# Kernel tuning notes

Measured on AMD Instinct MI355X. Metric: run time of the kernel, lower is better.

## Reference

```python
import jax, jax.numpy as jnp
import numpy as np

B, L, D = 2, 2048, 1536
H = 12            # num_heads == num_key_value_heads
FDIM = 16         # feature_dim (per-head q/k dim)
HD = D // H       # head_dim = 128 (per-head v dim)
EPS = 1e-12
W_STD = 0.02


def setup_inputs() -> dict:
    key = jax.random.key(0)
    k0, k1, k2, k3, k4 = jax.random.split(key, 5)
    hidden_states = jax.random.normal(k0, (B, L, D), dtype=jnp.float32)
    Wq = jax.random.normal(k1, (D, H * FDIM), dtype=jnp.float32) * W_STD
    Wk = jax.random.normal(k2, (D, H * FDIM), dtype=jnp.float32) * W_STD
    Wv = jax.random.normal(k3, (D, H * HD), dtype=jnp.float32) * W_STD
    Wo = jax.random.normal(k4, (H * HD, D), dtype=jnp.float32) * W_STD
    return {"hidden_states": hidden_states, "Wq": Wq, "Wk": Wk, "Wv": Wv, "Wo": Wo}


def _split_heads(x, h):
    b, l, hd = x.shape
    return x.reshape(b, l, h, hd // h).transpose(0, 2, 1, 3)  # b h l d


def reference(hidden_states, Wq, Wk, Wv, Wo):
    b, l, _ = hidden_states.shape
    q = _split_heads(hidden_states @ Wq, H)  # [b,h,l,FDIM]
    k = _split_heads(hidden_states @ Wk, H)  # [b,h,l,FDIM]
    v = _split_heads(hidden_states @ Wv, H)  # [b,h,l,HD]

    # parallel_based(q, k, v, eps, use_scale=True, use_normalize=True)
    q = q * (FDIM ** -0.5)
    s = jnp.einsum('bhld,bhmd->bhlm', q, k)            # raw qk scores
    attn = 1.0 + s + 0.5 * s * s                        # 2nd-order Taylor of exp
    causal = jnp.tril(jnp.ones((l, l), dtype=bool))
    attn = jnp.where(causal, attn, 0.0)
    o = jnp.einsum('bhlm,bhmd->bhld', attn, v)          # [b,h,l,HD]
    z = attn.sum(axis=-1)                               # causal normalizer [b,h,l]
    o = o / (z[..., None] + EPS)

    o = o.transpose(0, 2, 1, 3).reshape(b, l, H * HD)   # b l (h d)
    return o @ Wo
```

## Files before the change

kernel.cpp:

```cpp
#include <hip/hip_runtime.h>
#include <hip/hip_bf16.h>

typedef short short8 __attribute__((ext_vector_type(8)));
typedef float f32x4  __attribute__((ext_vector_type(4)));
typedef unsigned int u32x4 __attribute__((ext_vector_type(4)));

union V16   { u32x4 v; short8 s; };
union U16x8 { u32x4 v; unsigned short u[8]; };
union FB4   { u32x4 v; float f[4]; };
union BF2U  { __hip_bfloat162 h; unsigned int u; };

__device__ inline unsigned short f2bf(float f) {
  union { float f; unsigned int u; } x; x.f = f;
  unsigned int u = x.u + 0x7fffu + ((x.u >> 16) & 1u);
  return (unsigned short)(u >> 16);
}

__device__ __forceinline__ int probe_fp32(const unsigned short* hs) {
  int bad = 0;
#pragma unroll
  for (int i = 0; i < 64; ++i) {
    unsigned int e = (hs[2 * i] >> 7) & 0xFFu;
    if (e >= 0xFEu || (e > 0u && e < 0x60u)) bad++;
  }
  return bad >= 6;
}

__device__ __forceinline__ void gl_lds16(const unsigned short* g, unsigned short* l) {
  __builtin_amdgcn_global_load_lds(
      (const __attribute__((address_space(1))) unsigned int*)g,
      (__attribute__((address_space(3))) unsigned int*)l, 16, 0, 0);
}

__global__ __launch_bounds__(256) void w_tr(const void* __restrict__ Wq,
                                            const void* __restrict__ Wk,
                                            const void* __restrict__ Wv,
                                            const void* __restrict__ Wo,
                                            const void* __restrict__ hs,
                                            unsigned short* __restrict__ WT,
                                            unsigned short* __restrict__ WoT,
                                            unsigned short* __restrict__ hsb) {
  __shared__ unsigned short t[32][33];
  __shared__ int sf;
  if (threadIdx.x == 0) sf = probe_fp32((const unsigned short*)hs);
  __syncthreads();
  const int f = sf;
  const int z = blockIdx.z;
  if (z == 4) {
    size_t i0 = ((size_t)(blockIdx.y * 48 + blockIdx.x) * 256 + threadIdx.x) * 8;
    if (f) {
      const float* in = (const float*)hs;
      FB4 a, b; a.v = *(const u32x4*)&in[i0]; b.v = *(const u32x4*)&in[i0 + 4];
      U16x8 p;
#pragma unroll
      for (int j = 0; j < 4; ++j) { p.u[j] = f2bf(a.f[j]); p.u[j + 4] = f2bf(b.f[j]); }
      *(u32x4*)&hsb[i0] = p.v;
    } else {
      *(u32x4*)&hsb[i0] = *(const u32x4*)((const unsigned short*)hs + i0);
    }
    return;
  }
  if (blockIdx.y >= 48) return;
  const void* in_; unsigned short* out; int C;
  if      (z == 0) { in_ = Wq; out = WT;              C = 192;  }
  else if (z == 1) { in_ = Wk; out = WT + 192 * 1536; C = 192;  }
  else if (z == 2) { in_ = Wv; out = WT + 384 * 1536; C = 1536; }
  else             { in_ = Wo; out = WoT;             C = 1536; }
  const int c0 = blockIdx.x * 32;
  if (c0 >= C) return;
  const int tx = threadIdx.x & 31, ty = threadIdx.x >> 5;
  const int r0 = blockIdx.y * 32;
#pragma unroll
  for (int i = 0; i < 4; ++i) {
    size_t idx = (size_t)(r0 + ty + 8 * i) * C + (c0 + tx);
    t[ty + 8 * i][tx] = f ? f2bf(((const float*)in_)[idx])
                          : ((const unsigned short*)in_)[idx];
  }
  __syncthreads();
#pragma unroll
  for (int i = 0; i < 4; ++i)
    out[(size_t)(c0 + ty + 8 * i) * 1536 + (r0 + tx)] = t[tx][ty + 8 * i];
}

__global__ __launch_bounds__(256) void tr_v(const unsigned short* __restrict__ in_,
                                            unsigned short* __restrict__ out,
                                            int R, int C, int ldin,
                                            long long in_bstride, long long out_bstride) {
  __shared__ unsigned short t[32][33];
  const size_t ibase = (size_t)blockIdx.z * in_bstride;
  const size_t obase = (size_t)blockIdx.z * out_bstride;
  const int tx = threadIdx.x & 31, ty = threadIdx.x >> 5;
  const int r0 = blockIdx.y * 32, c0 = blockIdx.x * 32;
#pragma unroll
  for (int i = 0; i < 4; ++i)
    t[ty + 8 * i][tx] = in_[ibase + (size_t)(r0 + ty + 8 * i) * ldin + (c0 + tx)];
  __syncthreads();
#pragma unroll
  for (int i = 0; i < 4; ++i)
    out[obase + (size_t)(c0 + ty + 8 * i) * R + (r0 + tx)] = t[tx][ty + 8 * i];
}

__global__ __launch_bounds__(256) void gemm_bt(const unsigned short* __restrict__ A,
                                               const unsigned short* __restrict__ BT,
                                               void* __restrict__ C_,
                                               int M, int N, int K,
                                               const unsigned short* __restrict__ probe_src) {
  __shared__ unsigned short As[2][128][64];
  __shared__ unsigned short Bs[2][128][64];
  const int m0 = blockIdx.y * 128, n0 = blockIdx.x * 128;
  const int tid = threadIdx.x;
  const int lane = tid & 63, w = tid >> 6;
  const int wr = w >> 1, wc = w & 1;
  const int quad = lane >> 4, mrow = lane & 15;

  const int sr = lane >> 3;
  const int sc = ((lane & 7) ^ (lane >> 3)) * 8;
  const int fsw = (mrow & 7);

  const f32x4 zf = {0.f, 0.f, 0.f, 0.f};
  f32x4 acc[4][4];
#pragma unroll
  for (int mt = 0; mt < 4; ++mt)
#pragma unroll
    for (int nt = 0; nt < 4; ++nt) acc[mt][nt] = zf;

  const int nk = K >> 6;
#pragma unroll
  for (int j = 0; j < 4; ++j) {
    const int r = 32 * w + 8 * j + sr;
    gl_lds16(&A [(size_t)(m0 + r) * K + sc], &As[0][32 * w + 8 * j][0]);
    gl_lds16(&BT[(size_t)(n0 + r) * K + sc], &Bs[0][32 * w + 8 * j][0]);
  }

  for (int ks = 0; ks < nk; ++ks) {
    const int cur = ks & 1;
    __syncthreads();
    if (ks + 1 < nk) {
      const int k1 = (ks + 1) << 6;
#pragma unroll
      for (int j = 0; j < 4; ++j) {
        const int r = 32 * w + 8 * j + sr;
        gl_lds16(&A [(size_t)(m0 + r) * K + k1 + sc], &As[cur ^ 1][32 * w + 8 * j][0]);
        gl_lds16(&BT[(size_t)(n0 + r) * K + k1 + sc], &Bs[cur ^ 1][32 * w + 8 * j][0]);
      }
    }
#pragma unroll
    for (int kq = 0; kq < 2; ++kq) {
      short8 afr[4], bfr[4];
#pragma unroll
      for (int mt = 0; mt < 4; ++mt) {
        V16 u; u.v = *(const u32x4*)&As[cur][wr * 64 + mt * 16 + mrow][((kq * 4 + quad) ^ fsw) * 8];
        afr[mt] = u.s;
      }
#pragma unroll
      for (int nt = 0; nt < 4; ++nt) {
        V16 u; u.v = *(const u32x4*)&Bs[cur][wc * 64 + nt * 16 + mrow][((kq * 4 + quad) ^ fsw) * 8];
        bfr[nt] = u.s;
      }
#pragma unroll
      for (int mt = 0; mt < 4; ++mt)
#pragma unroll
        for (int nt = 0; nt < 4; ++nt)
          acc[mt][nt] = __builtin_amdgcn_mfma_f32_16x16x32_bf16(afr[mt], bfr[nt], acc[mt][nt], 0, 0, 0);
    }
  }

  const int of = probe_src ? probe_fp32(probe_src) : 0;
#pragma unroll
  for (int mt = 0; mt < 4; ++mt)
#pragma unroll
    for (int nt = 0; nt < 4; ++nt)
#pragma unroll
      for (int r = 0; r < 4; ++r) {
        int grow = m0 + wr * 64 + mt * 16 + quad * 4 + r;
        int gcol = n0 + wc * 64 + nt * 16 + mrow;
        size_t idx = (size_t)grow * N + gcol;
        if (of) ((float*)C_)[idx] = acc[mt][nt][r];
        else    ((unsigned short*)C_)[idx] = f2bf(acc[mt][nt][r]);
      }
}

__global__ __launch_bounds__(256, 3) void attn_based(const unsigned short* __restrict__ qkv,
                                                     const unsigned short* __restrict__ vT,
                                                     unsigned short* __restrict__ obuf) {
  __shared__ unsigned short Vs[2][128][64];
  const int LD = 1920;
  const int bh = blockIdx.x;
  const int qt = 31 - blockIdx.y;
  const int b = bh / 12, h = bh % 12;
  const int tid = threadIdx.x;
  const int lane = tid & 63, w = tid >> 6;
  const int quad = lane >> 4, mrow = lane & 15;
  const f32x4 zf = {0.f, 0.f, 0.f, 0.f};
  const bool act = (quad < 2);

  short8 bq = {0, 0, 0, 0, 0, 0, 0, 0};
  const int q_abs = qt * 64 + w * 16 + mrow;
  if (act) {
    V16 u; u.v = *(const u32x4*)&qkv[(size_t)(b * 2048 + q_abs) * LD + h * 16 + quad * 8];
    bq = u.s;
  }

  const int vr = lane >> 3;
  const int vc = ((lane & 7) ^ (lane >> 3)) * 8;
  const unsigned short* vbase = vT + (size_t)(bh * 128) * 2048;

  const unsigned short* kptr = &qkv[(size_t)(b * 2048 + mrow) * LD + 192 + h * 16 + quad * 8];

  f32x4 oacc[8];
#pragma unroll
  for (int nt = 0; nt < 8; ++nt) oacc[nt] = zf;
  float zcol = 0.f;

#pragma unroll
  for (int j = 0; j < 4; ++j)
    gl_lds16(vbase + (size_t)(32 * w + 8 * j + vr) * 2048 + vc, &Vs[0][32 * w + 8 * j][0]);
  V16 kf[4];
#pragma unroll
  for (int jt = 0; jt < 4; ++jt) {
    kf[jt].s = (short8){0, 0, 0, 0, 0, 0, 0, 0};
    if (act) kf[jt].v = *(const u32x4*)(kptr + (size_t)(jt * 16) * LD);
  }
  __syncthreads();

  for (int kt = 0; kt <= qt; ++kt) {
    const int kv0 = kt * 64;
    const int cur = kt & 1;
    if (kt < qt) {
#pragma unroll
      for (int j = 0; j < 4; ++j)
        gl_lds16(vbase + (size_t)(32 * w + 8 * j + vr) * 2048 + kv0 + 64 + vc,
                 &Vs[cur ^ 1][32 * w + 8 * j][0]);
    }

    f32x4 st[4];
#pragma unroll
    for (int jt = 0; jt < 4; ++jt)
      st[jt] = __builtin_amdgcn_mfma_f32_16x16x32_bf16(kf[jt].s, bq, zf, 0, 0, 0);

    kptr += (size_t)64 * LD;
    if (kt < qt) {
#pragma unroll
      for (int jt = 0; jt < 4; ++jt)
        if (act) kf[jt].v = *(const u32x4*)(kptr + (size_t)(jt * 16) * LD);
    }

    unsigned int pk[4][2];
#pragma unroll
    for (int jt = 0; jt < 4; ++jt) {
      const int kvb = kv0 + jt * 16 + quad * 4;
#pragma unroll
      for (int r2 = 0; r2 < 2; ++r2) {
        float s0 = st[jt][2 * r2], s1 = st[jt][2 * r2 + 1];
        float a0 = fmaf(s0, fmaf(s0, 0.03125f, 0.25f), 1.0f);
        float a1 = fmaf(s1, fmaf(s1, 0.03125f, 0.25f), 1.0f);
        a0 = (kvb + 2 * r2     <= q_abs) ? a0 : 0.0f;
        a1 = (kvb + 2 * r2 + 1 <= q_abs) ? a1 : 0.0f;
        zcol += a0 + a1;
        BF2U p; p.h = __float22bfloat162_rn(make_float2(a0, a1));
        pk[jt][r2] = p.u;
      }
    }
#pragma unroll
    for (int c = 0; c < 2; ++c) {
      union { short8 s; int wd[4]; } ap;
#pragma unroll
      for (int t = 0; t < 4; ++t) {
        int src = (2 * (quad & 1) + (t >> 1)) * 16 + mrow;
        int v0 = __shfl((int)pk[2 * c][t & 1], src, 64);
        int v1 = __shfl((int)pk[2 * c + 1][t & 1], src, 64);
        ap.wd[t] = (quad >> 1) ? v1 : v0;
      }
#pragma unroll
      for (int nt = 0; nt < 8; ++nt) {
        V16 u;
        u.v = *(const u32x4*)&Vs[cur][nt * 16 + mrow][((c * 4 + quad) ^ (mrow & 7)) * 8];
        oacc[nt] = __builtin_amdgcn_mfma_f32_16x16x32_bf16(ap.s, u.s, oacc[nt], 0, 0, 0);
      }
    }
    __syncthreads();
  }
  zcol += __shfl_xor(zcol, 16, 64);
  zcol += __shfl_xor(zcol, 32, 64);
  float inv[4];
#pragma unroll
  for (int r = 0; r < 4; ++r)
    inv[r] = 1.0f / (__shfl(zcol, quad * 4 + r, 64) + 1e-12f);
#pragma unroll
  for (int nt = 0; nt < 8; ++nt)
#pragma unroll
    for (int r = 0; r < 4; ++r)
      obuf[(size_t)(b * 2048 + qt * 64 + w * 16 + quad * 4 + r) * 1536 +
           h * 128 + nt * 16 + mrow] = f2bf(oacc[nt][r] * inv[r]);
}

extern "C" void kernel_launch(void* const* d_in, const int* in_sizes, int n_in,
                              void* d_out, int out_size, void* d_ws, size_t ws_size,
                              hipStream_t stream) {
  const void* hs = d_in[0];
  const void* Wq = d_in[1];
  const void* Wk = d_in[2];
  const void* Wv = d_in[3];
  const void* Wo = d_in[4];
  const unsigned short* hsp = (const unsigned short*)hs;

  unsigned short* ws   = (unsigned short*)d_ws;
  unsigned short* WT   = ws;
  unsigned short* WoT  = WT + 1920 * 1536;
  unsigned short* qkvb = WoT + 1536 * 1536;
  unsigned short* hsb  = qkvb + 4096 * 1920;
  unsigned short* vT   = hsb + 4096 * 1536;
  unsigned short* obuf = hsb;

  w_tr<<<dim3(48, 64, 5), 256, 0, stream>>>(Wq, Wk, Wv, Wo, hs, WT, WoT, hsb);

  gemm_bt<<<dim3(15, 32, 1), 256, 0, stream>>>(hsb, WT, qkvb, 4096, 1920, 1536, nullptr);

  tr_v<<<dim3(48, 64, 2), 256, 0, stream>>>(qkvb + 384, vT, 2048, 1536, 1920,
                                            (long long)2048 * 1920, (long long)1536 * 2048);

  attn_based<<<dim3(24, 32, 1), 256, 0, stream>>>(qkvb, vT, obuf);

  gemm_bt<<<dim3(12, 32, 1), 256, 0, stream>>>(obuf, WoT, d_out, 4096, 1536, 1536, hsp);
}
```

Baseline: 230.4 us.

## Rework attention kernel with 32x32 MFMA and split-KV waves with LDS reduction

The attention kernel now uses 32x32x16 bf16 MFMAs instead of 16x16x32. The four waves are split into two query halves by two KV halves, and partial outputs and normalizers are reduced through LDS at the end. The old version left half the lanes idle in the QK step and shuffled P across lanes; now every lane is used, P is rearranged with v_permlane32_swap, and the causal mask is applied only on the diagonal block. The cost is an extra LDS reduction and a sync at the end, plus s_setprio hints.

```diff
diff --git a/kernel.cpp b/kernel.cpp
--- a/kernel.cpp
+++ b/kernel.cpp
@@ -3,6 +3,7 @@
 
 typedef short short8 __attribute__((ext_vector_type(8)));
 typedef float f32x4  __attribute__((ext_vector_type(4)));
+typedef float f32x16 __attribute__((ext_vector_type(16)));
 typedef unsigned int u32x4 __attribute__((ext_vector_type(4)));
 
 union V16   { u32x4 v; short8 s; };
@@ -14,6 +15,14 @@
   union { float f; unsigned int u; } x; x.f = f;
   unsigned int u = x.u + 0x7fffu + ((x.u >> 16) & 1u);
   return (unsigned short)(u >> 16);
+}
+
+__device__ __forceinline__ unsigned int pkbf(float a, float b) {
+  BF2U p; p.h = __float22bfloat162_rn(make_float2(a, b)); return p.u;
+}
+
+__device__ __forceinline__ void plswap(unsigned int& a, unsigned int& b) {
+  asm("v_permlane32_swap_b32 %0, %1" : "+v"(a), "+v"(b));
 }
 
 __device__ __forceinline__ int probe_fp32(const unsigned short* hs) {
@@ -184,114 +193,149 @@
                                                      const unsigned short* __restrict__ vT,
                                                      unsigned short* __restrict__ obuf) {
   __shared__ unsigned short Vs[2][128][64];
+  __shared__ float zbuf[2][32];
   const int LD = 1920;
   const int bh = blockIdx.x;
   const int qt = 31 - blockIdx.y;
   const int b = bh / 12, h = bh % 12;
   const int tid = threadIdx.x;
   const int lane = tid & 63, w = tid >> 6;
-  const int quad = lane >> 4, mrow = lane & 15;
-  const f32x4 zf = {0.f, 0.f, 0.f, 0.f};
-  const bool act = (quad < 2);
-
-  short8 bq = {0, 0, 0, 0, 0, 0, 0, 0};
-  const int q_abs = qt * 64 + w * 16 + mrow;
-  if (act) {
-    V16 u; u.v = *(const u32x4*)&qkv[(size_t)(b * 2048 + q_abs) * LD + h * 16 + quad * 8];
-    bq = u.s;
-  }
-
-  const int vr = lane >> 3;
-  const int vc = ((lane & 7) ^ (lane >> 3)) * 8;
+  const int qsub = w & 1, kvp = w >> 1;
+  const int col = lane & 31, hi = lane >> 5;
+
+  const int q0 = qt * 64 + qsub * 32;
+  const int q_abs = q0 + col;
+
+  V16 bq; bq.v = *(const u32x4*)&qkv[(size_t)(b * 2048 + q_abs) * LD + h * 16 + hi * 8];
+
+  const unsigned short* kptr =
+      &qkv[(size_t)(b * 2048 + kvp * 32 + col) * LD + 192 + h * 16 + hi * 8];
+
   const unsigned short* vbase = vT + (size_t)(bh * 128) * 2048;
 
-  const unsigned short* kptr = &qkv[(size_t)(b * 2048 + mrow) * LD + 192 + h * 16 + quad * 8];
-
-  f32x4 oacc[8];
-#pragma unroll
-  for (int nt = 0; nt < 8; ++nt) oacc[nt] = zf;
-  float zcol = 0.f;
-
-#pragma unroll
-  for (int j = 0; j < 4; ++j)
-    gl_lds16(vbase + (size_t)(32 * w + 8 * j + vr) * 2048 + vc, &Vs[0][32 * w + 8 * j][0]);
-  V16 kf[4];
-#pragma unroll
-  for (int jt = 0; jt < 4; ++jt) {
-    kf[jt].s = (short8){0, 0, 0, 0, 0, 0, 0, 0};
-    if (act) kf[jt].v = *(const u32x4*)(kptr + (size_t)(jt * 16) * LD);
-  }
-  __syncthreads();
-
-  for (int kt = 0; kt <= qt; ++kt) {
-    const int kv0 = kt * 64;
-    const int cur = kt & 1;
-    if (kt < qt) {
-#pragma unroll
-      for (int j = 0; j < 4; ++j)
-        gl_lds16(vbase + (size_t)(32 * w + 8 * j + vr) * 2048 + kv0 + 64 + vc,
-                 &Vs[cur ^ 1][32 * w + 8 * j][0]);
-    }
-
-    f32x4 st[4];
-#pragma unroll
-    for (int jt = 0; jt < 4; ++jt)
-      st[jt] = __builtin_amdgcn_mfma_f32_16x16x32_bf16(kf[jt].s, bq, zf, 0, 0, 0);
-
+  const f32x16 z16 = {0.f,0.f,0.f,0.f,0.f,0.f,0.f,0.f,0.f,0.f,0.f,0.f,0.f,0.f,0.f,0.f};
+  f32x16 oacc[4];
+#pragma unroll
+  for (int nc = 0; nc < 4; ++nc) oacc[nc] = z16;
+  float zcA[4] = {0.f, 0.f, 0.f, 0.f};
+
+#define STAGE_V(KV0, BUF)                                                     \
+  {                                                                           \
+    _Pragma("unroll")                                                         \
+    for (int j = 0; j < 4; ++j) {                                             \
+      const int row = 32 * w + 8 * j + (lane >> 3);                           \
+      gl_lds16(vbase + (size_t)row * 2048 + (KV0) + ((lane & 7) ^ (lane >> 3)) * 8, \
+               &Vs[BUF][32 * w + 8 * j][0]);                                  \
+    }                                                                         \
+  }
+
+  STAGE_V(0, 0);
+  V16 kf; kf.v = *(const u32x4*)kptr;
+  __syncthreads();
+
+  for (int t = 0; t <= qt; ++t) {
+    const int cur = t & 1;
+    if (t < qt) STAGE_V((t + 1) * 64, cur ^ 1);
+
+    V16 kfn;
     kptr += (size_t)64 * LD;
-    if (kt < qt) {
-#pragma unroll
-      for (int jt = 0; jt < 4; ++jt)
-        if (act) kf[jt].v = *(const u32x4*)(kptr + (size_t)(jt * 16) * LD);
-    }
-
-    unsigned int pk[4][2];
-#pragma unroll
-    for (int jt = 0; jt < 4; ++jt) {
-      const int kvb = kv0 + jt * 16 + quad * 4;
-#pragma unroll
-      for (int r2 = 0; r2 < 2; ++r2) {
-        float s0 = st[jt][2 * r2], s1 = st[jt][2 * r2 + 1];
-        float a0 = fmaf(s0, fmaf(s0, 0.03125f, 0.25f), 1.0f);
-        float a1 = fmaf(s1, fmaf(s1, 0.03125f, 0.25f), 1.0f);
-        a0 = (kvb + 2 * r2     <= q_abs) ? a0 : 0.0f;
-        a1 = (kvb + 2 * r2 + 1 <= q_abs) ? a1 : 0.0f;
-        zcol += a0 + a1;
-        BF2U p; p.h = __float22bfloat162_rn(make_float2(a0, a1));
-        pk[jt][r2] = p.u;
-      }
-    }
-#pragma unroll
-    for (int c = 0; c < 2; ++c) {
-      union { short8 s; int wd[4]; } ap;
-#pragma unroll
-      for (int t = 0; t < 4; ++t) {
-        int src = (2 * (quad & 1) + (t >> 1)) * 16 + mrow;
-        int v0 = __shfl((int)pk[2 * c][t & 1], src, 64);
-        int v1 = __shfl((int)pk[2 * c + 1][t & 1], src, 64);
-        ap.wd[t] = (quad >> 1) ? v1 : v0;
-      }
-#pragma unroll
-      for (int nt = 0; nt < 8; ++nt) {
-        V16 u;
-        u.v = *(const u32x4*)&Vs[cur][nt * 16 + mrow][((c * 4 + quad) ^ (mrow & 7)) * 8];
-        oacc[nt] = __builtin_amdgcn_mfma_f32_16x16x32_bf16(ap.s, u.s, oacc[nt], 0, 0, 0);
-      }
+    if (t < qt) kfn.v = *(const u32x4*)kptr;
+
+    const bool live = (t < qt) | (kvp <= qsub);
+    if (live) {
+      f32x16 st = __builtin_amdgcn_mfma_f32_32x32x16_bf16(kf.s, bq.s, z16, 0, 0, 0);
+      const int kv0 = t * 64 + kvp * 32;
+      const bool diag = (t == qt) & (kvp == qsub);
+      float pr[16];
+      if (diag) {
+#pragma unroll
+        for (int r = 0; r < 16; ++r) {
+          float s = st[r];
+          float a = fmaf(s, fmaf(s, 0.03125f, 0.25f), 1.0f);
+          const int kvr = kv0 + (r & 3) + 8 * (r >> 2) + 4 * hi;
+          a = (kvr <= q_abs) ? a : 0.0f;
+          zcA[r & 3] += a; pr[r] = a;
+        }
+      } else {
+#pragma unroll
+        for (int r = 0; r < 16; ++r) {
+          float s = st[r];
+          float a = fmaf(s, fmaf(s, 0.03125f, 0.25f), 1.0f);
+          zcA[r & 3] += a; pr[r] = a;
+        }
+      }
+
+      union PA { short8 s; unsigned int wd[4]; } pa0, pa1;
+      {
+        unsigned int x0 = pkbf(pr[0], pr[1]), x1 = pkbf(pr[2], pr[3]);
+        unsigned int y0 = pkbf(pr[4], pr[5]), y1 = pkbf(pr[6], pr[7]);
+        plswap(x0, y0); plswap(x1, y1);
+        pa0.wd[0] = x0; pa0.wd[1] = x1; pa0.wd[2] = y0; pa0.wd[3] = y1;
+      }
+      {
+        unsigned int x0 = pkbf(pr[8], pr[9]),  x1 = pkbf(pr[10], pr[11]);
+        unsigned int y0 = pkbf(pr[12], pr[13]), y1 = pkbf(pr[14], pr[15]);
+        plswap(x0, y0); plswap(x1, y1);
+        pa1.wd[0] = x0; pa1.wd[1] = x1; pa1.wd[2] = y0; pa1.wd[3] = y1;
+      }
+
+      __builtin_amdgcn_s_setprio(1);
+#pragma unroll
+      for (int nc = 0; nc < 4; ++nc) {
+        const int hd = nc * 32 + col;
+        V16 v0, v1;
+        v0.v = *(const u32x4*)&Vs[cur][hd][(((kvp * 4 + hi)     ^ (hd & 7)) * 8)];
+        v1.v = *(const u32x4*)&Vs[cur][hd][(((kvp * 4 + 2 + hi) ^ (hd & 7)) * 8)];
+        oacc[nc] = __builtin_amdgcn_mfma_f32_32x32x16_bf16(pa0.s, v0.s, oacc[nc], 0, 0, 0);
+        oacc[nc] = __builtin_amdgcn_mfma_f32_32x32x16_bf16(pa1.s, v1.s, oacc[nc], 0, 0, 0);
+      }
+      __builtin_amdgcn_s_setprio(0);
     }
     __syncthreads();
-  }
-  zcol += __shfl_xor(zcol, 16, 64);
+    if (t < qt) kf = kfn;
+  }
+
+  float zcol = (zcA[0] + zcA[1]) + (zcA[2] + zcA[3]);
   zcol += __shfl_xor(zcol, 32, 64);
-  float inv[4];
-#pragma unroll
-  for (int r = 0; r < 4; ++r)
-    inv[r] = 1.0f / (__shfl(zcol, quad * 4 + r, 64) + 1e-12f);
-#pragma unroll
-  for (int nt = 0; nt < 8; ++nt)
-#pragma unroll
-    for (int r = 0; r < 4; ++r)
-      obuf[(size_t)(b * 2048 + qt * 64 + w * 16 + quad * 4 + r) * 1536 +
-           h * 128 + nt * 16 + mrow] = f2bf(oacc[nt][r] * inv[r]);
+
+  float* fbuf = (float*)&Vs[0][0][0];
+  if (w >= 2) {
+    const int base = (w & 1) * 4096;
+#pragma unroll
+    for (int nc = 0; nc < 4; ++nc)
+#pragma unroll
+      for (int g = 0; g < 4; ++g) {
+        f32x4 v = {oacc[nc][4 * g], oacc[nc][4 * g + 1],
+                   oacc[nc][4 * g + 2], oacc[nc][4 * g + 3]};
+        *(f32x4*)&fbuf[base + ((nc * 4 + g) * 64 + lane) * 4] = v;
+      }
+    if (lane < 32) zbuf[w & 1][lane] = zcol;
+  }
+  __syncthreads();
+  if (w < 2) {
+    const int base = w * 4096;
+#pragma unroll
+    for (int nc = 0; nc < 4; ++nc)
+#pragma unroll
+      for (int g = 0; g < 4; ++g) {
+        f32x4 v = *(const f32x4*)&fbuf[base + ((nc * 4 + g) * 64 + lane) * 4];
+#pragma unroll
+        for (int r = 0; r < 4; ++r) oacc[nc][4 * g + r] += v[r];
+      }
+    const float zinv = 1.0f / (zcol + zbuf[w][col] + 1e-12f);
+#pragma unroll
+    for (int g = 0; g < 4; ++g)
+#pragma unroll
+      for (int rr = 0; rr < 4; ++rr) {
+        const int qrow = rr + 8 * g + 4 * hi;
+        const float iv = __shfl(zinv, qrow, 64);
+        const size_t base_o = (size_t)(b * 2048 + q0 + qrow) * 1536 + h * 128 + col;
+#pragma unroll
+        for (int nc = 0; nc < 4; ++nc)
+          obuf[base_o + nc * 32] = f2bf(oacc[nc][4 * g + rr] * iv);
+      }
+  }
+#undef STAGE_V
 }
 
 extern "C" void kernel_launch(void* const* d_in, const int* in_sizes, int n_in,
```

Result: faster. 223.2 us (-3.1%).
